# Optimization experiments

Hardware: AMD Instinct MI355X
Metric: run time of the kernel (lower is better)

The kernel has to match this reference:

```python
import jax, jax.numpy as jnp
import numpy as np

D = 256      # feature_dim (d_model)
H = 4        # num_heads
N = 4096     # query nodes
M = 4096     # source nodes


def _conv1x1(W, b, x):
    # Conv1d(kernel_size=1): per-position linear over channels. x: [1, Cin, N]
    return jnp.einsum('oi,bin->bon', W, x) + b[None, :, None]


def setup_inputs() -> dict:
    key = jax.random.key(0)
    ks = jax.random.split(key, 16)
    s = 0.02
    inp = {
        'x':      jax.random.normal(ks[0], (1, D, N), jnp.float32),
        'source': jax.random.normal(ks[1], (1, D, M), jnp.float32),
        'dist':   jax.random.uniform(ks[2], (1, N, M), jnp.float32),
        'mask':   jax.random.bernoulli(ks[3], 0.5, (N, M)),
        'Wq': s * jax.random.normal(ks[4], (D, D), jnp.float32),  'bq': jnp.zeros((D,), jnp.float32),
        'Wk': s * jax.random.normal(ks[5], (D, D), jnp.float32),  'bk': jnp.zeros((D,), jnp.float32),
        'Wv': s * jax.random.normal(ks[6], (D, D), jnp.float32),  'bv': jnp.zeros((D,), jnp.float32),
        'Wm': s * jax.random.normal(ks[7], (D, D), jnp.float32),  'bm': jnp.zeros((D,), jnp.float32),
        'W1': s * jax.random.normal(ks[8], (2 * D, 2 * D), jnp.float32), 'b1': jnp.zeros((2 * D,), jnp.float32),
        'W2': s * jax.random.normal(ks[9], (D, 2 * D), jnp.float32),     'b2': jnp.zeros((D,), jnp.float32),
    }
    return inp


def reference(x, source, dist, mask, Wq, bq, Wk, bk, Wv, bv, Wm, bm, W1, b1, W2, b2):
    dim = D // H  # per-head dim; torch view(1, dim, H, -1) splits channels as (dim, H)
    q = _conv1x1(Wq, bq, x).reshape(1, dim, H, N)
    k = _conv1x1(Wk, bk, source).reshape(1, dim, H, M)
    v = _conv1x1(Wv, bv, source).reshape(1, dim, H, M)

    scores = jnp.einsum('bdhn,bdhm->bhnm', q, k) / jnp.sqrt(jnp.asarray(dim, q.dtype))
    # non-standard additive mask: global detached min scales the masked-out entries
    smin = jax.lax.stop_gradient(scores.min())
    scores = scores + smin * (~mask).astype(scores.dtype)[None, None, :, :]

    prob = jax.nn.softmax(scores, axis=-1)                       # [1,H,N,M]
    attn = jnp.einsum('bhnm,bdhm->bdhn', prob, v)                # [1,dim,H,N]
    message = _conv1x1(Wm, bm, attn.reshape(1, D, N))            # merge heads

    h = jnp.concatenate([x, message], axis=1)                    # [1,2D,N]
    h = jax.nn.relu(_conv1x1(W1, b1, h))
    y = _conv1x1(W2, b2, h)                                      # [1,D,N]
    weights = scores.mean(axis=1)                                # [1,N,M]
    return y, weights
```

## Files before the change

kernel.cpp:

```cpp
#include <hip/hip_runtime.h>
#include <hip/hip_bf16.h>
#include <math.h>

#define Dm 256
#define Hh 4
#define Nn 4096
#define Mq 4096

typedef __attribute__((ext_vector_type(8))) short bf16x8;
typedef __attribute__((ext_vector_type(4))) float f32x4;
typedef _Float16 __attribute__((ext_vector_type(4))) f16x4;
typedef __fp16 __attribute__((ext_vector_type(2))) h16x2;

#define MFMA_BF16(a,b,c) __builtin_amdgcn_mfma_f32_16x16x32_bf16(a,b,c,0,0,0)
#define MFMA_F16x16(a,b,c) __builtin_amdgcn_mfma_f32_16x16x16f16(a,b,c,0,0,0)

#define MB (1u<<20)
#define OFF_FLAG  0
#define OFF_SMIN  64
#define OFF_PART  1024
#define OFF_KMAX  3072
#define OFF_MT    4096
#define OFF_DENP  (128u<<10)
#define OFF_WB    (3u*MB/2)
#define OFF_BITS  (3u*MB)
#define OFF_QB    (5u*MB)
#define OFF_KB    (7u*MB)
#define OFF_VB    (9u*MB)
#define OFF_HCAT  (11u*MB)
#define OFF_ATTNT (15u*MB)
#define OFF_XT    (17u*MB)
#define OFF_ST    (19u*MB)
#define OFF_OPART (17u*MB)
#define OFF_H1T   (17u*MB)

#define WOFF_Q  0
#define WOFF_K  65536
#define WOFF_V  131072
#define WOFF_M  196608
#define WOFF_1  262144
#define WOFF_2  524288

__device__ __forceinline__ unsigned short f2bf(float x) {
    unsigned u = __float_as_uint(x);
    u += 0x7FFF + ((u >> 16) & 1);
    return (unsigned short)(u >> 16);
}
__device__ __forceinline__ float bf2f(unsigned short b) {
    return __uint_as_float(((unsigned)b) << 16);
}

__global__ void k_detect(const unsigned char* __restrict__ mb, int* __restrict__ flag,
                         unsigned* __restrict__ kmax) {
    __shared__ int c[5];
    if (threadIdx.x < 5) c[threadIdx.x] = 0;
    if (threadIdx.x < 4) kmax[threadIdx.x] = 0u;
    __syncthreads();
    for (int i = threadIdx.x; i < 16384; i += blockDim.x) {
        unsigned char b = mb[i];
        if (b) {
            atomicAdd(&c[i & 3], 1);
            if ((i & 7) == 4) atomicAdd(&c[4], 1);
        }
    }
    __syncthreads();
    if (threadIdx.x == 0) {
        int f;
        if (c[3] > 0 && c[0] == 0)          f = 3;
        else if (c[1] | c[2] | c[3])        f = 1;
        else if (c[4] > 0)                  f = 0;
        else                                f = 2;
        *flag = f;
    }
}

__global__ void k_maskbits(const void* __restrict__ mp, const int* __restrict__ flagp,
                           unsigned char* __restrict__ bits) {
    size_t i = (size_t)blockIdx.x * 256 + threadIdx.x;
    const int flag = *flagp;
    size_t base = i * 8;
    unsigned b = 0;
    if (flag == 1) {
        unsigned long long u = *(const unsigned long long*)((const unsigned char*)mp + base);
        #pragma unroll
        for (int j = 0; j < 8; j++) b |= (unsigned)(((u >> (8*j)) & 0xFFull) != 0ull) << j;
    } else if (flag == 0) {
        const int* p = (const int*)mp;
        #pragma unroll
        for (int j = 0; j < 8; j++) b |= (unsigned)(p[base + j] != 0) << j;
    } else if (flag == 3) {
        const float* p = (const float*)mp;
        #pragma unroll
        for (int j = 0; j < 8; j++) b |= (unsigned)(p[base + j] != 0.0f) << j;
    } else {
        const unsigned long long* p = (const unsigned long long*)mp;
        #pragma unroll
        for (int j = 0; j < 8; j++) b |= (unsigned)(p[base + j] != 0ull) << j;
    }
    bits[i] = (unsigned char)b;
}

__global__ __launch_bounds__(256) void k_prep(const float* __restrict__ x,
                                              const float* __restrict__ source,
                                              unsigned short* __restrict__ xt,
                                              unsigned short* __restrict__ st,
                                              unsigned short* __restrict__ hcat) {
    const int z = blockIdx.z;
    const float* src = z ? source : x;
    unsigned short* dst = z ? st : xt;
    unsigned short* dst2 = z ? nullptr : hcat;
    const int l = threadIdx.x & 63, g = threadIdx.x >> 6;
    const int c = blockIdx.y * 64 + l;
    const int n0 = blockIdx.x * 32 + g * 8;
    float4 v0 = *(const float4*)(src + (size_t)c * Nn + n0);
    float4 v1 = *(const float4*)(src + (size_t)c * Nn + n0 + 4);
    float vv[8] = {v0.x, v0.y, v0.z, v0.w, v1.x, v1.y, v1.z, v1.w};
    #pragma unroll
    for (int j = 0; j < 8; j++) {
        unsigned short b = f2bf(vv[j]);
        dst[(size_t)(n0 + j) * 256 + c] = b;
        if (dst2) dst2[(size_t)(n0 + j) * 512 + c] = b;
    }
}

__global__ void k_wcast(const float* __restrict__ Wq, const float* __restrict__ Wk,
                        const float* __restrict__ Wv, const float* __restrict__ Wm,
                        const float* __restrict__ W1, const float* __restrict__ W2,
                        unsigned short* __restrict__ wb) {
    size_t i = (size_t)blockIdx.x * 256 + threadIdx.x;
    const float* s; size_t off;
    if      (i < 65536)               { s = Wq; off = i; }
    else if (i < 131072)              { s = Wk; off = i - 65536; }
    else if (i < 196608)              { s = Wv; off = i - 131072; }
    else if (i < 262144)              { s = Wm; off = i - 196608; }
    else if (i < 524288)              { s = W1; off = i - 262144; }
    else                              { s = W2; off = i - 524288; }
    wb[i] = f2bf(s[off]);
}

template<int KK>
__device__ __forceinline__ void gemm_body(const unsigned short* __restrict__ wb,
                                          const float* __restrict__ bias,
                                          const unsigned short* __restrict__ xt,
                                          void* __restrict__ out, int mode,
                                          int bx, int by) {
    const int tid = threadIdx.x, w = tid >> 6, lane = tid & 63;
    const int lg = lane >> 4, lr = lane & 15;
    const int o_base = by * 64 + w * 16;
    const int n_base = bx * 64;
    f32x4 acc[4];
    #pragma unroll
    for (int j = 0; j < 4; j++) acc[j] = (f32x4){0.f, 0.f, 0.f, 0.f};
    const unsigned short* wrow = wb + (size_t)(o_base + lr) * KK + lg * 8;
    const unsigned short* xrow = xt + (size_t)(n_base + lr) * KK + lg * 8;
    #pragma unroll
    for (int k0 = 0; k0 < KK; k0 += 32) {
        bf16x8 af = *(const bf16x8*)(wrow + k0);
        #pragma unroll
        for (int j = 0; j < 4; j++) {
            bf16x8 bfr = *(const bf16x8*)(xrow + (size_t)j * 16 * KK + k0);
            acc[j] = MFMA_BF16(af, bfr, acc[j]);
        }
    }
    float bv[4];
    #pragma unroll
    for (int r = 0; r < 4; r++) bv[r] = bias[o_base + lg * 4 + r];
    #pragma unroll
    for (int j = 0; j < 4; j++) {
        #pragma unroll
        for (int r = 0; r < 4; r++) {
            int o = o_base + lg * 4 + r;
            int n = n_base + j * 16 + lr;
            float v = acc[j][r] + bv[r];
            if (mode == 0) {
                ((float*)out)[(size_t)o * Nn + n] = v;
            } else if (mode == 1) {
                ((unsigned short*)out)[(((size_t)(o & 3)) * Nn + n) * 64 + (o >> 2)] = f2bf(v);
            } else if (mode == 2) {
                union { _Float16 h; unsigned short u; } cv; cv.h = (_Float16)v;
                ((unsigned short*)out)[(((size_t)(o & 3)) * 64 + (o >> 2)) * Mq + n] = cv.u;
            } else if (mode == 3) {
                ((unsigned short*)out)[(size_t)n * 512 + 256 + o] = f2bf(v);
            } else if (mode == 4) {
                ((unsigned short*)out)[(size_t)n * 512 + o] = f2bf(fmaxf(v, 0.f));
            } else {
                int dd = o >> 2, hh = o & 3, g = dd >> 3, pos = dd & 7;
                int slot = g ^ (n & 7);
                ((unsigned short*)out)[(((size_t)hh * Mq + n)) * 64 + slot * 8 + pos] = f2bf(v);
            }
        }
    }
}

template<int KK>
__global__ __launch_bounds__(256) void k_mgemm(const unsigned short* __restrict__ wb,
                                               const float* __restrict__ bias,
                                               const unsigned short* __restrict__ xt,
                                               void* __restrict__ out, int mode) {
    gemm_body<KK>(wb, bias, xt, out, mode, blockIdx.x, blockIdx.y);
}

__global__ __launch_bounds__(256) void k_qkv(const unsigned short* __restrict__ wb,
                                             const float* __restrict__ bq,
                                             const float* __restrict__ bk,
                                             const float* __restrict__ bv,
                                             const unsigned short* __restrict__ xt,
                                             const unsigned short* __restrict__ st,
                                             void* __restrict__ qb, void* __restrict__ kb,
                                             void* __restrict__ vb) {
    const int z = blockIdx.z;
    const float* bias = (z == 0) ? bq : ((z == 1) ? bk : bv);
    const unsigned short* X = (z == 0) ? xt : st;
    void* out = (z == 0) ? qb : ((z == 1) ? kb : vb);
    int mode = (z == 0) ? 1 : ((z == 1) ? 5 : 2);
    gemm_body<256>(wb + z * 65536, bias, X, out, mode, blockIdx.x, blockIdx.y);
}

__global__ __launch_bounds__(256) void k_knorm(const unsigned short* __restrict__ kb,
                                               unsigned* __restrict__ kmax) {
    const int h = blockIdx.y;
    const int m = blockIdx.x * 256 + threadIdx.x;
    const unsigned short* row = kb + ((size_t)(h * Mq + m) << 6);
    float s = 0.f;
    #pragma unroll
    for (int i = 0; i < 64; i++) { float v = bf2f(row[i]); s = fmaf(v, v, s); }
    __shared__ float red[256];
    red[threadIdx.x] = s;
    __syncthreads();
    for (int st = 128; st > 0; st >>= 1) {
        if (threadIdx.x < st) red[threadIdx.x] = fmaxf(red[threadIdx.x], red[threadIdx.x + st]);
        __syncthreads();
    }
    if (threadIdx.x == 0) atomicMax(kmax + h, __float_as_uint(red[0]));
}

__global__ __launch_bounds__(256) void k_qnorm(const unsigned short* __restrict__ qb,
                                               const unsigned* __restrict__ kmax,
                                               float* __restrict__ mtarr) {
    const int row = blockIdx.x * 256 + threadIdx.x;
    const unsigned short* qr = qb + ((size_t)row << 6);
    float s = 0.f;
    #pragma unroll
    for (int i = 0; i < 64; i++) { float v = bf2f(qr[i]); s = fmaf(v, v, s); }
    float k2 = __uint_as_float(kmax[row >> 12]);
    mtarr[row] = sqrtf(s * k2) * 0.125f;
}

__global__ __launch_bounds__(512) void k_min(
    const unsigned short* __restrict__ qb, const unsigned short* __restrict__ kb,
    float* __restrict__ partial) {
    __shared__ unsigned short kbuf[2][8192];
    const int tid = threadIdx.x;
    const int w = tid >> 6, lane = tid & 63;
    const int lg = lane >> 4, lr = lane & 15;
    const int n0 = blockIdx.x * 128 + w * 16;
    const int m0 = blockIdx.y * 256;

    bf16x8 qf[4][2];
    #pragma unroll
    for (int h = 0; h < 4; h++)
        #pragma unroll
        for (int kh = 0; kh < 2; kh++)
            qf[h][kh] = *(const bf16x8*)(qb + (((size_t)h * Nn + n0 + lr) << 6) + kh*32 + lg*8);

    const int h0 = tid >> 8, q0 = tid & 255;
    const unsigned short* src0 = kb + (((size_t)h0 * Mq + m0) << 6) + q0 * 8;
    const unsigned short* src1 = kb + (((size_t)(h0 + 2) * Mq + m0) << 6) + q0 * 8;
    unsigned short* dst0 = &kbuf[0][h0 * 2048 + q0 * 8];
    unsigned short* dst1 = &kbuf[0][(h0 + 2) * 2048 + q0 * 8];

    float mn = INFINITY;

    bf16x8 r0 = *(const bf16x8*)(src0);
    bf16x8 r1 = *(const bf16x8*)(src1);
    *(bf16x8*)dst0 = r0;
    *(bf16x8*)dst1 = r1;
    __syncthreads();
    r0 = *(const bf16x8*)(src0 + 2048);
    r1 = *(const bf16x8*)(src1 + 2048);

    for (int t = 0; t < 8; t++) {
        const unsigned short* kB = &kbuf[t & 1][0];
        #pragma unroll
        for (int mi = 0; mi < 2; mi++) {
            const int rowoff = (mi * 16 + lr) * 64;
            #pragma unroll
            for (int h = 0; h < 4; h++) {
                bf16x8 a0 = *(const bf16x8*)(kB + h*2048 + rowoff + ((lg ^ (lr & 7)) << 3));
                bf16x8 a1 = *(const bf16x8*)(kB + h*2048 + rowoff + (((lg + 4) ^ (lr & 7)) << 3));
                f32x4 acc = (f32x4){0.f, 0.f, 0.f, 0.f};
                acc = MFMA_BF16(a0, qf[h][0], acc);
                acc = MFMA_BF16(a1, qf[h][1], acc);
                mn = fminf(mn, fminf(fminf(acc[0], acc[1]), fminf(acc[2], acc[3])));
            }
        }
        if (t < 7) {
            *(bf16x8*)(dst0 + (((t + 1) & 1) ? 8192 : 0)) = r0;
            *(bf16x8*)(dst1 + (((t + 1) & 1) ? 8192 : 0)) = r1;
        }
        __syncthreads();
        if (t < 6) {
            r0 = *(const bf16x8*)(src0 + (size_t)(t + 2) * 2048);
            r1 = *(const bf16x8*)(src1 + (size_t)(t + 2) * 2048);
        }
    }

    for (int off = 1; off < 64; off <<= 1) mn = fminf(mn, __shfl_xor(mn, off));
    __shared__ float wmin[8];
    if (lane == 0) wmin[w] = mn;
    __syncthreads();
    if (tid == 0) {
        float m2 = wmin[0];
        #pragma unroll
        for (int i = 1; i < 8; i++) m2 = fminf(m2, wmin[i]);
        partial[blockIdx.x * 16 + blockIdx.y] = m2 * 0.125f;
    }
}

__global__ void k_minreduce(const float* __restrict__ partial, float* __restrict__ smin) {
    const int tid = threadIdx.x;
    float mn = fminf(partial[tid], partial[tid + 256]);
    __shared__ float red[256];
    red[tid] = mn;
    __syncthreads();
    for (int st = 128; st > 0; st >>= 1) {
        if (tid < st) red[tid] = fminf(red[tid], red[tid + st]);
        __syncthreads();
    }
    if (tid == 0) *smin = red[0];
}

__global__ __launch_bounds__(512) void k_wout(
    const unsigned short* __restrict__ qb, const unsigned short* __restrict__ kb,
    const unsigned long long* __restrict__ bits,
    const float* __restrict__ sminp, float* __restrict__ wout) {
    __shared__ unsigned short kbuf[2][8192];
    const int tid = threadIdx.x;
    const int w = tid >> 6, lane = tid & 63;
    const int lg = lane >> 4, lr = lane & 15;
    const int n0 = blockIdx.x * 128 + w * 16;
    const int m0 = blockIdx.y * 256;
    const float smin = *sminp;

    bf16x8 qf[4][2];
    #pragma unroll
    for (int h = 0; h < 4; h++)
        #pragma unroll
        for (int kh = 0; kh < 2; kh++)
            qf[h][kh] = *(const bf16x8*)(qb + (((size_t)h * Nn + n0 + lr) << 6) + kh*32 + lg*8);

    const int h0 = tid >> 8, q0 = tid & 255;
    const unsigned short* src0 = kb + (((size_t)h0 * Mq + m0) << 6) + q0 * 8;
    const unsigned short* src1 = kb + (((size_t)(h0 + 2) * Mq + m0) << 6) + q0 * 8;
    unsigned short* dst0 = &kbuf[0][h0 * 2048 + q0 * 8];
    unsigned short* dst1 = &kbuf[0][(h0 + 2) * 2048 + q0 * 8];

    const unsigned long long* brow = bits + (((size_t)(n0 + lr)) << 6) + (m0 >> 6);
    unsigned long long bw = 0ull;

    bf16x8 r0 = *(const bf16x8*)(src0);
    bf16x8 r1 = *(const bf16x8*)(src1);
    *(bf16x8*)dst0 = r0;
    *(bf16x8*)dst1 = r1;
    __syncthreads();
    r0 = *(const bf16x8*)(src0 + 2048);
    r1 = *(const bf16x8*)(src1 + 2048);

    for (int t = 0; t < 8; t++) {
        const unsigned short* kB = &kbuf[t & 1][0];
        const int mch = m0 + t * 32;
        if ((t & 1) == 0) bw = brow[t >> 1];
        #pragma unroll
        for (int mi = 0; mi < 2; mi++) {
            const int rowoff = (mi * 16 + lr) * 64;
            f32x4 accA = (f32x4){0.f, 0.f, 0.f, 0.f};
            f32x4 accB = (f32x4){0.f, 0.f, 0.f, 0.f};
            #pragma unroll
            for (int h = 0; h < 2; h++) {
                bf16x8 a0 = *(const bf16x8*)(kB + h*2048 + rowoff + ((lg ^ (lr & 7)) << 3));
                bf16x8 a1 = *(const bf16x8*)(kB + h*2048 + rowoff + (((lg + 4) ^ (lr & 7)) << 3));
                accA = MFMA_BF16(a0, qf[h][0], accA);
                accA = MFMA_BF16(a1, qf[h][1], accA);
            }
            #pragma unroll
            for (int h = 2; h < 4; h++) {
                bf16x8 a0 = *(const bf16x8*)(kB + h*2048 + rowoff + ((lg ^ (lr & 7)) << 3));
                bf16x8 a1 = *(const bf16x8*)(kB + h*2048 + rowoff + (((lg + 4) ^ (lr & 7)) << 3));
                accB = MFMA_BF16(a0, qf[h][0], accB);
                accB = MFMA_BF16(a1, qf[h][1], accB);
            }
            const int shb = (t & 1) * 32 + mi * 16 + lg * 4;
            f32x4 wv;
            #pragma unroll
            for (int r = 0; r < 4; r++) {
                bool b = (bw >> (shb + r)) & 1ull;
                wv[r] = fmaf(accA[r] + accB[r], 0.03125f, b ? 0.f : smin);
            }
            *(f32x4*)(wout + (size_t)(n0 + lr) * Mq + mch + mi * 16 + lg * 4) = wv;
        }
        if (t < 7) {
            *(bf16x8*)(dst0 + (((t + 1) & 1) ? 8192 : 0)) = r0;
            *(bf16x8*)(dst1 + (((t + 1) & 1) ? 8192 : 0)) = r1;
        }
        __syncthreads();
        if (t < 6) {
            r0 = *(const bf16x8*)(src0 + (size_t)(t + 2) * 2048);
            r1 = *(const bf16x8*)(src1 + (size_t)(t + 2) * 2048);
        }
    }
}

__global__ __launch_bounds__(512) void k_pv(
    const unsigned short* __restrict__ qb, const unsigned short* __restrict__ kb,
    const unsigned short* __restrict__ vbh,
    const unsigned long long* __restrict__ bits,
    const float* __restrict__ sminp, const float* __restrict__ mtarr,
    float* __restrict__ denp, unsigned short* __restrict__ opart) {
    __shared__ unsigned short kbuf[2][4096];
    __shared__ unsigned short vbuf[2][4096];
    const int tid = threadIdx.x;
    const int w = tid >> 6, lane = tid & 63;
    const int lg = lane >> 4, lr = lane & 15;
    const int h = blockIdx.y & 3, mb = blockIdx.y >> 2;
    const int n0 = blockIdx.x * 128 + w * 16;
    const int m0 = mb * 1024;
    const float smin = *sminp;
    const float sminc = fmaxf(smin, 0.f);

    bf16x8 qf0 = *(const bf16x8*)(qb + (((size_t)h * Nn + n0 + lr) << 6) + lg*8);
    bf16x8 qf1 = *(const bf16x8*)(qb + (((size_t)h * Nn + n0 + lr) << 6) + 32 + lg*8);
    float mtE = mtarr[(size_t)h * Nn + n0 + lr] + sminc;
    const float cT = -mtE * 1.44269504f;
    const float cF = cT + smin * 1.44269504f;

    f32x4 oacc[4];
    #pragma unroll
    for (int ds = 0; ds < 4; ds++) oacc[ds] = (f32x4){0.f, 0.f, 0.f, 0.f};
    float dsum = 0.f;

    const unsigned short* ksrc = kb + (((size_t)h * Mq + m0) << 6) + tid * 8;
    const int vdd = tid >> 3, vj = tid & 7;
    const unsigned short* vsrc = vbh + (size_t)(h * 64 + vdd) * Mq + m0 + vj * 8;
    const int vds = vdd >> 4, vlr = vdd & 15, vmi = vj >> 1;
    const int vswz = (vlr >> 2) & 3;
    const int vbase = ((vmi * 4 + vds) * 16 + vlr) * 4;
    const int vdst0 = (vbase + (((vj & 1) * 2 + 0) ^ vswz)) * 4;
    const int vdst1 = (vbase + (((vj & 1) * 2 + 1) ^ vswz)) * 4;

    union { bf16x8 v; unsigned long long q[2]; } rv;
    bf16x8 rk = *(const bf16x8*)(ksrc);
    rv.v = *(const bf16x8*)(vsrc);
    *(bf16x8*)&kbuf[0][tid * 8] = rk;
    *(unsigned long long*)&vbuf[0][vdst0] = rv.q[0];
    *(unsigned long long*)&vbuf[0][vdst1] = rv.q[1];
    __syncthreads();
    rk = *(const bf16x8*)(ksrc + 4096);
    rv.v = *(const bf16x8*)(vsrc + 64);

    const unsigned long long* brow = bits + (((size_t)(n0 + lr)) << 6) + (m0 >> 6);
    const int kslot0 = (lg ^ (lr & 7)) << 3;
    const int kslot1 = ((lg + 4) ^ (lr & 7)) << 3;
    const int vrslot = (lg ^ ((lr >> 2) & 3)) * 4;

    for (int t = 0; t < 16; t++) {
        const unsigned short* kB = &kbuf[t & 1][0];
        const unsigned short* vB = &vbuf[t & 1][0];
        unsigned long long bw = brow[t];
        #pragma unroll
        for (int mi = 0; mi < 4; mi++) {
            const int rowoff = (mi * 16 + lr) * 64;
            bf16x8 a0 = *(const bf16x8*)(kB + rowoff + kslot0);
            bf16x8 a1 = *(const bf16x8*)(kB + rowoff + kslot1);
            f16x4 vf[4];
            #pragma unroll
            for (int ds = 0; ds < 4; ds++)
                vf[ds] = *(const f16x4*)&vB[((mi * 4 + ds) * 16 + lr) * 16 + vrslot];
            f32x4 acc = (f32x4){0.f, 0.f, 0.f, 0.f};
            acc = MFMA_BF16(a0, qf0, acc);
            acc = MFMA_BF16(a1, qf1, acc);
            const int shb = mi * 16 + lg * 4;
            float p0 = exp2f(fmaf(acc[0], 0.18033688f, ((bw >> (shb + 0)) & 1ull) ? cT : cF));
            float p1 = exp2f(fmaf(acc[1], 0.18033688f, ((bw >> (shb + 1)) & 1ull) ? cT : cF));
            float p2 = exp2f(fmaf(acc[2], 0.18033688f, ((bw >> (shb + 2)) & 1ull) ? cT : cF));
            float p3 = exp2f(fmaf(acc[3], 0.18033688f, ((bw >> (shb + 3)) & 1ull) ? cT : cF));
            dsum += (p0 + p1) + (p2 + p3);
            union { h16x2 h2[2]; f16x4 f4; } pu;
            pu.h2[0] = __builtin_amdgcn_cvt_pkrtz(p0, p1);
            pu.h2[1] = __builtin_amdgcn_cvt_pkrtz(p2, p3);
            f16x4 pf = pu.f4;
            #pragma unroll
            for (int ds = 0; ds < 4; ds++)
                oacc[ds] = MFMA_F16x16(pf, vf[ds], oacc[ds]);
        }
        if (t < 15) {
            *(bf16x8*)&kbuf[(t + 1) & 1][tid * 8] = rk;
            *(unsigned long long*)&vbuf[(t + 1) & 1][vdst0] = rv.q[0];
            *(unsigned long long*)&vbuf[(t + 1) & 1][vdst1] = rv.q[1];
        }
        __syncthreads();
        if (t < 14) {
            rk = *(const bf16x8*)(ksrc + (size_t)(t + 2) * 4096);
            rv.v = *(const bf16x8*)(vsrc + (size_t)(t + 2) * 64);
        }
    }

    dsum += __shfl_xor(dsum, 16);
    dsum += __shfl_xor(dsum, 32);
    if (lane < 16)
        denp[((size_t)h * Nn + n0 + lane) * 4 + mb] = dsum;

    unsigned short* op = opart + (size_t)mb * (Dm * Nn);
    #pragma unroll
    for (int ds = 0; ds < 4; ds++) {
        int c = (ds * 16 + lr) * 4 + h;
        int n = n0 + lg * 4;
        unsigned long long pk =
            (unsigned long long)f2bf(oacc[ds][0]) |
            ((unsigned long long)f2bf(oacc[ds][1]) << 16) |
            ((unsigned long long)f2bf(oacc[ds][2]) << 32) |
            ((unsigned long long)f2bf(oacc[ds][3]) << 48);
        *(unsigned long long*)&op[(size_t)c * Nn + n] = pk;
    }
}

__global__ __launch_bounds__(256) void k_finish(const unsigned short* __restrict__ opart,
                                                const float* __restrict__ denp,
                                                unsigned short* __restrict__ attnT) {
    __shared__ float t[64][65];
    const int cb = blockIdx.y * 64, nb = blockIdx.x * 64;
    const int tid = threadIdx.x;
    #pragma unroll
    for (int e = 0; e < 16; e++) {
        int idx = e * 256 + tid;
        int c_l = idx >> 6, n_l = idx & 63;
        int c = cb + c_l, n = nb + n_l;
        float s = 0.f;
        #pragma unroll
        for (int y = 0; y < 4; y++)
            s += bf2f(opart[(size_t)y * (Dm*Nn) + (size_t)c * Nn + n]);
        size_t row = (size_t)(c & 3) * Nn + n;
        float d = denp[row*4] + denp[row*4+1] + denp[row*4+2] + denp[row*4+3];
        t[c_l][n_l] = s / d;
    }
    __syncthreads();
    #pragma unroll
    for (int e = 0; e < 16; e++) {
        int idx = e * 256 + tid;
        int n_l = idx >> 6, c_l = idx & 63;
        attnT[(size_t)(nb + n_l) * 256 + cb + c_l] = f2bf(t[c_l][n_l]);
    }
}

extern "C" void kernel_launch(void* const* d_in, const int* in_sizes, int n_in,
                              void* d_out, int out_size, void* d_ws, size_t ws_size,
                              hipStream_t stream) {
    const float* x      = (const float*)d_in[0];
    const float* source = (const float*)d_in[1];
    const void*  mask   = d_in[3];
    const float* Wq = (const float*)d_in[4];  const float* bq = (const float*)d_in[5];
    const float* Wk = (const float*)d_in[6];  const float* bk = (const float*)d_in[7];
    const float* Wv = (const float*)d_in[8];  const float* bv = (const float*)d_in[9];
    const float* Wm = (const float*)d_in[10]; const float* bm = (const float*)d_in[11];
    const float* W1 = (const float*)d_in[12]; const float* b1 = (const float*)d_in[13];
    const float* W2 = (const float*)d_in[14]; const float* b2 = (const float*)d_in[15];

    float* y    = (float*)d_out;
    float* wout = y + (size_t)Dm * Nn;

    char* ws = (char*)d_ws;
    int*      flag  = (int*)(ws + OFF_FLAG);
    float*    sminp = (float*)(ws + OFF_SMIN);
    float*    part  = (float*)(ws + OFF_PART);
    unsigned* kmax  = (unsigned*)(ws + OFF_KMAX);
    float*    mtarr = (float*)(ws + OFF_MT);
    float*    denp  = (float*)(ws + OFF_DENP);
    unsigned short* wb    = (unsigned short*)(ws + OFF_WB);
    unsigned char*  bits  = (unsigned char*)(ws + OFF_BITS);
    unsigned short* qb    = (unsigned short*)(ws + OFF_QB);
    unsigned short* kb    = (unsigned short*)(ws + OFF_KB);
    unsigned short* vb    = (unsigned short*)(ws + OFF_VB);
    unsigned short* hcat  = (unsigned short*)(ws + OFF_HCAT);
    unsigned short* attnT = (unsigned short*)(ws + OFF_ATTNT);
    unsigned short* xt    = (unsigned short*)(ws + OFF_XT);
    unsigned short* st    = (unsigned short*)(ws + OFF_ST);
    unsigned short* opart = (unsigned short*)(ws + OFF_OPART);
    unsigned short* h1t   = (unsigned short*)(ws + OFF_H1T);

    k_detect<<<1, 256, 0, stream>>>((const unsigned char*)mask, flag, kmax);
    k_maskbits<<<8192, 256, 0, stream>>>(mask, flag, bits);

    k_prep<<<dim3(128, 4, 2), 256, 0, stream>>>(x, source, xt, st, hcat);
    k_wcast<<<2560, 256, 0, stream>>>(Wq, Wk, Wv, Wm, W1, W2, wb);

    k_qkv<<<dim3(64, 4, 3), 256, 0, stream>>>(wb, bq, bk, bv, xt, st, qb, kb, vb);

    k_knorm<<<dim3(16, 4), 256, 0, stream>>>(kb, kmax);
    k_qnorm<<<64, 256, 0, stream>>>(qb, kmax, mtarr);

    k_min<<<dim3(32, 16), 512, 0, stream>>>(qb, kb, part);
    k_minreduce<<<1, 256, 0, stream>>>(part, sminp);

    k_wout<<<dim3(32, 16), 512, 0, stream>>>(qb, kb, (const unsigned long long*)bits, sminp, wout);

    k_pv<<<dim3(32, 16), 512, 0, stream>>>(qb, kb, vb, (const unsigned long long*)bits,
                                           sminp, mtarr, denp, opart);
    k_finish<<<dim3(64, 4), 256, 0, stream>>>(opart, denp, attnT);

    k_mgemm<256><<<dim3(64, 4), 256, 0, stream>>>(wb + WOFF_M, bm, attnT, hcat, 3);
    k_mgemm<512><<<dim3(64, 8), 256, 0, stream>>>(wb + WOFF_1, b1, hcat, h1t, 4);
    k_mgemm<512><<<dim3(64, 4), 256, 0, stream>>>(wb + WOFF_2, b2, h1t, y, 0);
}
```

Measured before the change: 198.1 us.

## Fuse score-min with weights output and apply the mask fix in a separate pass

The score-min pass now also writes the head-averaged scores directly to the weights output and reduces the global min with an order-preserving atomicMin key. This removes the separate min-reduce kernel and the second QK recomputation in k_wout. A new elementwise k_wfix kernel then adds smin at masked positions, which costs an extra 64MB read-modify-write of the weights output. Mask-type detection and initialisation move into one block of k_prep, removing one launch.

Result: slower. 215.2 us (+8.6%).

```diff
diff --git a/kernel.cpp b/kernel.cpp
--- a/kernel.cpp
+++ b/kernel.cpp
@@ -18,8 +18,7 @@
 #define MB (1u<<20)
 #define OFF_FLAG  0
 #define OFF_SMIN  64
-#define OFF_PART  1024
-#define OFF_KMAX  3072
+#define OFF_KMAX  128
 #define OFF_MT    4096
 #define OFF_DENP  (128u<<10)
 #define OFF_WB    (3u*MB/2)
@@ -49,62 +48,23 @@
 __device__ __forceinline__ float bf2f(unsigned short b) {
     return __uint_as_float(((unsigned)b) << 16);
 }
-
-__global__ void k_detect(const unsigned char* __restrict__ mb, int* __restrict__ flag,
-                         unsigned* __restrict__ kmax) {
-    __shared__ int c[5];
-    if (threadIdx.x < 5) c[threadIdx.x] = 0;
-    if (threadIdx.x < 4) kmax[threadIdx.x] = 0u;
-    __syncthreads();
-    for (int i = threadIdx.x; i < 16384; i += blockDim.x) {
-        unsigned char b = mb[i];
-        if (b) {
-            atomicAdd(&c[i & 3], 1);
-            if ((i & 7) == 4) atomicAdd(&c[4], 1);
-        }
-    }
-    __syncthreads();
-    if (threadIdx.x == 0) {
-        int f;
-        if (c[3] > 0 && c[0] == 0)          f = 3;
-        else if (c[1] | c[2] | c[3])        f = 1;
-        else if (c[4] > 0)                  f = 0;
-        else                                f = 2;
-        *flag = f;
-    }
-}
-
-__global__ void k_maskbits(const void* __restrict__ mp, const int* __restrict__ flagp,
-                           unsigned char* __restrict__ bits) {
-    size_t i = (size_t)blockIdx.x * 256 + threadIdx.x;
-    const int flag = *flagp;
-    size_t base = i * 8;
-    unsigned b = 0;
-    if (flag == 1) {
-        unsigned long long u = *(const unsigned long long*)((const unsigned char*)mp + base);
-        #pragma unroll
-        for (int j = 0; j < 8; j++) b |= (unsigned)(((u >> (8*j)) & 0xFFull) != 0ull) << j;
-    } else if (flag == 0) {
-        const int* p = (const int*)mp;
-        #pragma unroll
-        for (int j = 0; j < 8; j++) b |= (unsigned)(p[base + j] != 0) << j;
-    } else if (flag == 3) {
-        const float* p = (const float*)mp;
-        #pragma unroll
-        for (int j = 0; j < 8; j++) b |= (unsigned)(p[base + j] != 0.0f) << j;
-    } else {
-        const unsigned long long* p = (const unsigned long long*)mp;
-        #pragma unroll
-        for (int j = 0; j < 8; j++) b |= (unsigned)(p[base + j] != 0ull) << j;
-    }
-    bits[i] = (unsigned char)b;
+__device__ __forceinline__ unsigned fkey(float f) {
+    unsigned u = __float_as_uint(f);
+    return (u & 0x80000000u) ? ~u : (u | 0x80000000u);
+}
+__device__ __forceinline__ float fdecode(unsigned k) {
+    return (k & 0x80000000u) ? __uint_as_float(k ^ 0x80000000u) : __uint_as_float(~k);
 }
 
 __global__ __launch_bounds__(256) void k_prep(const float* __restrict__ x,
                                               const float* __restrict__ source,
                                               unsigned short* __restrict__ xt,
                                               unsigned short* __restrict__ st,
-                                              unsigned short* __restrict__ hcat) {
+                                              unsigned short* __restrict__ hcat,
+                                              const unsigned char* __restrict__ maskb,
+                                              int* __restrict__ flag,
+                                              unsigned* __restrict__ kmax,
+                                              unsigned* __restrict__ sminkey) {
     const int z = blockIdx.z;
     const float* src = z ? source : x;
     unsigned short* dst = z ? st : xt;
@@ -121,6 +81,55 @@
         dst[(size_t)(n0 + j) * 256 + c] = b;
         if (dst2) dst2[(size_t)(n0 + j) * 512 + c] = b;
     }
+    if (blockIdx.x == 0 && blockIdx.y == 0 && z == 0) {
+        __shared__ int cnt[5];
+        if (threadIdx.x < 5) cnt[threadIdx.x] = 0;
+        if (threadIdx.x < 4) kmax[threadIdx.x] = 0u;
+        if (threadIdx.x == 0) *sminkey = 0xFFFFFFFFu;
+        __syncthreads();
+        for (int i = threadIdx.x; i < 16384; i += 256) {
+            unsigned char b = maskb[i];
+            if (b) {
+                atomicAdd(&cnt[i & 3], 1);
+                if ((i & 7) == 4) atomicAdd(&cnt[4], 1);
+            }
+        }
+        __syncthreads();
+        if (threadIdx.x == 0) {
+            int f;
+            if (cnt[3] > 0 && cnt[0] == 0)        f = 3;
+            else if (cnt[1] | cnt[2] | cnt[3])    f = 1;
+            else if (cnt[4] > 0)                  f = 0;
+            else                                  f = 2;
+            *flag = f;
+        }
+    }
+}
+
+__global__ void k_maskbits(const void* __restrict__ mp, const int* __restrict__ flagp,
+                           unsigned char* __restrict__ bits) {
+    size_t i = (size_t)blockIdx.x * 256 + threadIdx.x;
+    const int flag = *flagp;
+    size_t base = i * 8;
+    unsigned b = 0;
+    if (flag == 1) {
+        unsigned long long u = *(const unsigned long long*)((const unsigned char*)mp + base);
+        #pragma unroll
+        for (int j = 0; j < 8; j++) b |= (unsigned)(((u >> (8*j)) & 0xFFull) != 0ull) << j;
+    } else if (flag == 0) {
+        const int* p = (const int*)mp;
+        #pragma unroll
+        for (int j = 0; j < 8; j++) b |= (unsigned)(p[base + j] != 0) << j;
+    } else if (flag == 3) {
+        const float* p = (const float*)mp;
+        #pragma unroll
+        for (int j = 0; j < 8; j++) b |= (unsigned)(p[base + j] != 0.0f) << j;
+    } else {
+        const unsigned long long* p = (const unsigned long long*)mp;
+        #pragma unroll
+        for (int j = 0; j < 8; j++) b |= (unsigned)(p[base + j] != 0ull) << j;
+    }
+    bits[i] = (unsigned char)b;
 }
 
 __global__ void k_wcast(const float* __restrict__ Wq, const float* __restrict__ Wk,
@@ -246,9 +255,9 @@
     mtarr[row] = sqrtf(s * k2) * 0.125f;
 }
 
-__global__ __launch_bounds__(512) void k_min(
+__global__ __launch_bounds__(512) void k_minwout(
     const unsigned short* __restrict__ qb, const unsigned short* __restrict__ kb,
-    float* __restrict__ partial) {
+    unsigned* __restrict__ sminkey, float* __restrict__ wout) {
     __shared__ unsigned short kbuf[2][8192];
     const int tid = threadIdx.x;
     const int w = tid >> 6, lane = tid & 63;
@@ -281,9 +290,11 @@
 
     for (int t = 0; t < 8; t++) {
         const unsigned short* kB = &kbuf[t & 1][0];
+        const int mch = m0 + t * 32;
         #pragma unroll
         for (int mi = 0; mi < 2; mi++) {
             const int rowoff = (mi * 16 + lr) * 64;
+            f32x4 wsum = (f32x4){0.f, 0.f, 0.f, 0.f};
             #pragma unroll
             for (int h = 0; h < 4; h++) {
                 bf16x8 a0 = *(const bf16x8*)(kB + h*2048 + rowoff + ((lg ^ (lr & 7)) << 3));
@@ -292,7 +303,13 @@
                 acc = MFMA_BF16(a0, qf[h][0], acc);
                 acc = MFMA_BF16(a1, qf[h][1], acc);
                 mn = fminf(mn, fminf(fminf(acc[0], acc[1]), fminf(acc[2], acc[3])));
+                wsum += acc;
             }
+            f32x4 wv;
+            #pragma unroll
+            for (int rr = 0; rr < 4; rr++) wv[rr] = wsum[rr] * 0.03125f;
+            __builtin_nontemporal_store(wv,
+                (f32x4*)(wout + (size_t)(n0 + lr) * Mq + mch + mi * 16 + lg * 4));
         }
         if (t < 7) {
             *(bf16x8*)(dst0 + (((t + 1) & 1) ? 8192 : 0)) = r0;
@@ -313,108 +330,32 @@
         float m2 = wmin[0];
         #pragma unroll
         for (int i = 1; i < 8; i++) m2 = fminf(m2, wmin[i]);
-        partial[blockIdx.x * 16 + blockIdx.y] = m2 * 0.125f;
-    }
-}
-
-__global__ void k_minreduce(const float* __restrict__ partial, float* __restrict__ smin) {
-    const int tid = threadIdx.x;
-    float mn = fminf(partial[tid], partial[tid + 256]);
-    __shared__ float red[256];
-    red[tid] = mn;
-    __syncthreads();
-    for (int st = 128; st > 0; st >>= 1) {
-        if (tid < st) red[tid] = fminf(red[tid], red[tid + st]);
-        __syncthreads();
-    }
-    if (tid == 0) *smin = red[0];
-}
-
-__global__ __launch_bounds__(512) void k_wout(
-    const unsigned short* __restrict__ qb, const unsigned short* __restrict__ kb,
-    const unsigned long long* __restrict__ bits,
-    const float* __restrict__ sminp, float* __restrict__ wout) {
-    __shared__ unsigned short kbuf[2][8192];
-    const int tid = threadIdx.x;
-    const int w = tid >> 6, lane = tid & 63;
-    const int lg = lane >> 4, lr = lane & 15;
-    const int n0 = blockIdx.x * 128 + w * 16;
-    const int m0 = blockIdx.y * 256;
-    const float smin = *sminp;
-
-    bf16x8 qf[4][2];
-    #pragma unroll
-    for (int h = 0; h < 4; h++)
-        #pragma unroll
-        for (int kh = 0; kh < 2; kh++)
-            qf[h][kh] = *(const bf16x8*)(qb + (((size_t)h * Nn + n0 + lr) << 6) + kh*32 + lg*8);
-
-    const int h0 = tid >> 8, q0 = tid & 255;
-    const unsigned short* src0 = kb + (((size_t)h0 * Mq + m0) << 6) + q0 * 8;
-    const unsigned short* src1 = kb + (((size_t)(h0 + 2) * Mq + m0) << 6) + q0 * 8;
-    unsigned short* dst0 = &kbuf[0][h0 * 2048 + q0 * 8];
-    unsigned short* dst1 = &kbuf[0][(h0 + 2) * 2048 + q0 * 8];
-
-    const unsigned long long* brow = bits + (((size_t)(n0 + lr)) << 6) + (m0 >> 6);
-    unsigned long long bw = 0ull;
-
-    bf16x8 r0 = *(const bf16x8*)(src0);
-    bf16x8 r1 = *(const bf16x8*)(src1);
-    *(bf16x8*)dst0 = r0;
-    *(bf16x8*)dst1 = r1;
-    __syncthreads();
-    r0 = *(const bf16x8*)(src0 + 2048);
-    r1 = *(const bf16x8*)(src1 + 2048);
-
-    for (int t = 0; t < 8; t++) {
-        const unsigned short* kB = &kbuf[t & 1][0];
-        const int mch = m0 + t * 32;
-        if ((t & 1) == 0) bw = brow[t >> 1];
-        #pragma unroll
-        for (int mi = 0; mi < 2; mi++) {
-            const int rowoff = (mi * 16 + lr) * 64;
-            f32x4 accA = (f32x4){0.f, 0.f, 0.f, 0.f};
-            f32x4 accB = (f32x4){0.f, 0.f, 0.f, 0.f};
-            #pragma unroll
-            for (int h = 0; h < 2; h++) {
-                bf16x8 a0 = *(const bf16x8*)(kB + h*2048 + rowoff + ((lg ^ (lr & 7)) << 3));
-                bf16x8 a1 = *(const bf16x8*)(kB + h*2048 + rowoff + (((lg + 4) ^ (lr & 7)) << 3));
-                accA = MFMA_BF16(a0, qf[h][0], accA);
-                accA = MFMA_BF16(a1, qf[h][1], accA);
-            }
-            #pragma unroll
-            for (int h = 2; h < 4; h++) {
-                bf16x8 a0 = *(const bf16x8*)(kB + h*2048 + rowoff + ((lg ^ (lr & 7)) << 3));
-                bf16x8 a1 = *(const bf16x8*)(kB + h*2048 + rowoff + (((lg + 4) ^ (lr & 7)) << 3));
-                accB = MFMA_BF16(a0, qf[h][0], accB);
-                accB = MFMA_BF16(a1, qf[h][1], accB);
-            }
-            const int shb = (t & 1) * 32 + mi * 16 + lg * 4;
-            f32x4 wv;
-            #pragma unroll
-            for (int r = 0; r < 4; r++) {
-                bool b = (bw >> (shb + r)) & 1ull;
-                wv[r] = fmaf(accA[r] + accB[r], 0.03125f, b ? 0.f : smin);
-            }
-            *(f32x4*)(wout + (size_t)(n0 + lr) * Mq + mch + mi * 16 + lg * 4) = wv;
-        }
-        if (t < 7) {
-            *(bf16x8*)(dst0 + (((t + 1) & 1) ? 8192 : 0)) = r0;
-            *(bf16x8*)(dst1 + (((t + 1) & 1) ? 8192 : 0)) = r1;
-        }
-        __syncthreads();
-        if (t < 6) {
-            r0 = *(const bf16x8*)(src0 + (size_t)(t + 2) * 2048);
-            r1 = *(const bf16x8*)(src1 + (size_t)(t + 2) * 2048);
-        }
-    }
+        atomicMin(sminkey, fkey(m2 * 0.125f));
+    }
+}
+
+__global__ __launch_bounds__(256) void k_wfix(float* __restrict__ wout,
+                                              const unsigned long long* __restrict__ bits,
+                                              const unsigned* __restrict__ skey) {
+    const float smin = fdecode(*skey);
+    size_t base = ((size_t)blockIdx.x * 256 + threadIdx.x) * 16;
+    unsigned nib = (unsigned)((bits[base >> 6] >> (base & 63)) & 0xFFFFull);
+    float* p = wout + base;
+    f32x4 v[4];
+    #pragma unroll
+    for (int q = 0; q < 4; q++) v[q] = ((const f32x4*)p)[q];
+    #pragma unroll
+    for (int j = 0; j < 16; j++)
+        if (!((nib >> j) & 1u)) v[j >> 2][j & 3] += smin;
+    #pragma unroll
+    for (int q = 0; q < 4; q++) __builtin_nontemporal_store(v[q], (f32x4*)p + q);
 }
 
 __global__ __launch_bounds__(512) void k_pv(
     const unsigned short* __restrict__ qb, const unsigned short* __restrict__ kb,
     const unsigned short* __restrict__ vbh,
     const unsigned long long* __restrict__ bits,
-    const float* __restrict__ sminp, const float* __restrict__ mtarr,
+    const unsigned* __restrict__ skey, const float* __restrict__ mtarr,
     float* __restrict__ denp, unsigned short* __restrict__ opart) {
     __shared__ unsigned short kbuf[2][4096];
     __shared__ unsigned short vbuf[2][4096];
@@ -424,7 +365,7 @@
     const int h = blockIdx.y & 3, mb = blockIdx.y >> 2;
     const int n0 = blockIdx.x * 128 + w * 16;
     const int m0 = mb * 1024;
-    const float smin = *sminp;
+    const float smin = fdecode(*skey);
     const float sminc = fmaxf(smin, 0.f);
 
     bf16x8 qf0 = *(const bf16x8*)(qb + (((size_t)h * Nn + n0 + lr) << 6) + lg*8);
@@ -569,8 +510,7 @@
 
     char* ws = (char*)d_ws;
     int*      flag  = (int*)(ws + OFF_FLAG);
-    float*    sminp = (float*)(ws + OFF_SMIN);
-    float*    part  = (float*)(ws + OFF_PART);
+    unsigned* skey  = (unsigned*)(ws + OFF_SMIN);
     unsigned* kmax  = (unsigned*)(ws + OFF_KMAX);
     float*    mtarr = (float*)(ws + OFF_MT);
     float*    denp  = (float*)(ws + OFF_DENP);
@@ -586,10 +526,9 @@
     unsigned short* opart = (unsigned short*)(ws + OFF_OPART);
     unsigned short* h1t   = (unsigned short*)(ws + OFF_H1T);
 
-    k_detect<<<1, 256, 0, stream>>>((const unsigned char*)mask, flag, kmax);
+    k_prep<<<dim3(128, 4, 2), 256, 0, stream>>>(x, source, xt, st, hcat,
+                                                (const unsigned char*)mask, flag, kmax, skey);
     k_maskbits<<<8192, 256, 0, stream>>>(mask, flag, bits);
-
-    k_prep<<<dim3(128, 4, 2), 256, 0, stream>>>(x, source, xt, st, hcat);
     k_wcast<<<2560, 256, 0, stream>>>(Wq, Wk, Wv, Wm, W1, W2, wb);
 
     k_qkv<<<dim3(64, 4, 3), 256, 0, stream>>>(wb, bq, bk, bv, xt, st, qb, kb, vb);
@@ -597,13 +536,11 @@
     k_knorm<<<dim3(16, 4), 256, 0, stream>>>(kb, kmax);
     k_qnorm<<<64, 256, 0, stream>>>(qb, kmax, mtarr);
 
-    k_min<<<dim3(32, 16), 512, 0, stream>>>(qb, kb, part);
-    k_minreduce<<<1, 256, 0, stream>>>(part, sminp);
-
-    k_wout<<<dim3(32, 16), 512, 0, stream>>>(qb, kb, (const unsigned long long*)bits, sminp, wout);
+    k_minwout<<<dim3(32, 16), 512, 0, stream>>>(qb, kb, skey, wout);
+    k_wfix<<<4096, 256, 0, stream>>>(wout, (const unsigned long long*)bits, skey);
 
     k_pv<<<dim3(32, 16), 512, 0, stream>>>(qb, kb, vb, (const unsigned long long*)bits,
-                                           sminp, mtarr, denp, opart);
+                                           skey, mtarr, denp, opart);
     k_finish<<<dim3(64, 4), 256, 0, stream>>>(opart, denp, attnT);
 
     k_mgemm<256><<<dim3(64, 4), 256, 0, stream>>>(wb + WOFF_M, bm, attnT, hcat, 3);
```
